# Optimization experiments

Measured on AMD Instinct MI355X. Metric: run time of the kernel, lower is better.

The kernel has to match this reference:

```python
import jax, jax.numpy as jnp
import numpy as np

NUM_HEADS = 8
NUM_LEVELS = 4
NUM_POINTS = 4


def setup_inputs() -> dict:
    key = jax.random.key(0)
    kq, kp, kv, k1, k2, k3, k4 = jax.random.split(key, 7)
    B, Q, C = 4, 4096, 256
    M, L, P = NUM_HEADS, NUM_LEVELS, NUM_POINTS
    shapes_np = np.array([[128, 128], [64, 64], [32, 32], [16, 16]], dtype=np.int32)
    sizes = shapes_np[:, 0] * shapes_np[:, 1]
    N = int(sizes.sum())  # 21760
    level_index = jnp.asarray(np.concatenate([[0], np.cumsum(sizes)[:-1]]).astype(np.int32))
    q = jax.random.normal(kq, (B, Q, C), jnp.float32)
    p = jax.random.uniform(kp, (B, Q, L, 2), jnp.float32)  # normalized ref points
    v = jax.random.normal(kv, (B, N, C), jnp.float32)
    # proj_offset bias: radial grid init from reset_parameters()
    t = np.arange(M, dtype=np.float32) * (2.0 * np.pi / M)
    grid = np.stack([np.cos(t), np.sin(t)], -1)
    grid = grid / np.abs(grid).max(-1, keepdims=True)
    grid = np.tile(grid[:, None, None, :], (1, L, P, 1)) * np.arange(1, P + 1, dtype=np.float32)[None, None, :, None]
    b_off = jnp.asarray(grid.reshape(-1))
    s = 1.0 / np.sqrt(C).astype(np.float32)
    W_off = jax.random.normal(k1, (C, M * L * P * 2), jnp.float32) * 0.01
    W_attn = jax.random.normal(k2, (C, M * L * P), jnp.float32) * s
    b_attn = jnp.zeros((M * L * P,), jnp.float32)
    W_val = jax.random.normal(k3, (C, C), jnp.float32) * s
    b_val = jnp.zeros((C,), jnp.float32)
    W_out = jax.random.normal(k4, (C, C), jnp.float32) * s
    b_out = jnp.zeros((C,), jnp.float32)
    return {"q": q, "p": p, "v": v, "shapes": jnp.asarray(shapes_np), "level_index": level_index,
            "W_off": W_off, "b_off": b_off, "W_attn": W_attn, "b_attn": b_attn,
            "W_val": W_val, "b_val": b_val, "W_out": W_out, "b_out": b_out}


def _ms_deform_attn(q, p, v, shapes, level_index, W_off, b_off, W_attn, b_attn, W_val, b_val, W_out, b_out):
    B, Q, C = q.shape
    M, L, P = NUM_HEADS, NUM_LEVELS, NUM_POINTS
    D = C // M
    N = v.shape[1]
    # value projection -> [B, M, N, D] (head-major for gather)
    v_p = (v @ W_val + b_val).reshape(B, N, M, D).transpose(0, 2, 1, 3)
    # attention weights, softmax over L*P (classic MSDeformAttn kernel contract)
    attn = jax.nn.softmax((q @ W_attn + b_attn).reshape(B, Q, M, L * P), axis=-1)
    attn = attn.reshape(B, Q, M, L, P)
    # sampling locations (P==2 reference-point branch)
    off = (q @ W_off + b_off).reshape(B, Q, M, L, P, 2)
    norm = jnp.stack([shapes[:, 1], shapes[:, 0]], -1).astype(jnp.float32)  # (W, H) per level
    loc = p[:, :, None, :, None, :] + off / norm[None, None, None, :, None, :]  # [B,Q,M,L,P,2]

    out = jnp.zeros((B, M, Q, D), jnp.float32)
    for l in range(L):
        Hf = shapes[l, 0].astype(jnp.float32)
        Wf = shapes[l, 1].astype(jnp.float32)
        Hi = shapes[l, 0]
        Wi = shapes[l, 1]
        base = level_index[l]
        # grid_sample(align_corners=False) convention: pixel = loc*size - 0.5
        x = loc[:, :, :, l, :, 0] * Wf - 0.5  # [B,Q,M,P]
        y = loc[:, :, :, l, :, 1] * Hf - 0.5
        x0 = jnp.floor(x)
        y0 = jnp.floor(y)
        lx, ly = x - x0, y - y0
        x0i = x0.astype(jnp.int32)
        y0i = y0.astype(jnp.int32)

        def corner(xi, yi, w):
            valid = (xi >= 0) & (xi < Wi) & (yi >= 0) & (yi < Hi)
            idx = base + jnp.clip(yi, 0, Hi - 1) * Wi + jnp.clip(xi, 0, Wi - 1)  # [B,Q,M,P]
            idx = idx.transpose(0, 2, 1, 3).reshape(B, M, Q * P)
            g = jnp.take_along_axis(v_p, idx[..., None], axis=2).reshape(B, M, Q, P, D)
            wv = (w * valid.astype(w.dtype)).transpose(0, 2, 1, 3)[..., None]  # [B,M,Q,P,1]
            return g * wv

        samp = (corner(x0i, y0i, (1 - lx) * (1 - ly))
                + corner(x0i + 1, y0i, lx * (1 - ly))
                + corner(x0i, y0i + 1, (1 - lx) * ly)
                + corner(x0i + 1, y0i + 1, lx * ly))  # [B,M,Q,P,D]
        a_l = attn[:, :, :, l, :].transpose(0, 2, 1, 3)  # [B,M,Q,P]
        out = out + jnp.einsum('bmqpd,bmqp->bmqd', samp, a_l)

    out = out.transpose(0, 2, 1, 3).reshape(B, Q, M * D)
    return out @ W_out + b_out


def reference(q, p, v, shapes, level_index, W_off, b_off, W_attn, b_attn, W_val, b_val, W_out, b_out):
    return _ms_deform_attn(q, p, v, shapes, level_index, W_off, b_off, W_attn, b_attn, W_val, b_val, W_out, b_out)
```

## Files before the change

### kernel.cpp

```cpp
#include <hip/hip_runtime.h>
#include <cstddef>

#define BB 4
#define QQ 4096
#define MM 8
#define NN 21760

typedef __bf16 bf16_8 __attribute__((ext_vector_type(8)));
typedef __bf16 bf16_4 __attribute__((ext_vector_type(4)));
typedef float  floatx4 __attribute__((ext_vector_type(4)));

__global__ __launch_bounds__(256) void prep_weights(
    const float* __restrict__ Wv, const float* __restrict__ Wa,
    const float* __restrict__ Wo, const float* __restrict__ Wu,
    const float* __restrict__ ba, const float* __restrict__ bo,
    __bf16* __restrict__ Wt, float* __restrict__ biasq)
{
    const int gid = blockIdx.x * 256 + threadIdx.x;
    if (gid < 65536) {
        const int n = gid >> 8, k = gid & 255;
        Wt[gid] = (__bf16)Wv[k * 256 + n];
    } else if (gid < 163840) {
        const int o = gid - 65536;
        const int n = o >> 8, k = o & 255;
        Wt[gid] = (__bf16)(n < 128 ? Wa[k * 128 + n] : Wo[k * 256 + (n - 128)]);
    } else if (gid < 229376) {
        const int o = gid - 163840;
        const int n = o >> 8, k = o & 255;
        Wt[gid] = (__bf16)Wu[k * 256 + n];
    } else if (gid < 229760) {
        const int j = gid - 229376;
        biasq[j] = (j < 128) ? ba[j] : bo[j - 128];
    }
}

template<typename AT, int NCOLS, int MODE, int TILES>
__global__ __launch_bounds__(512) void gemm_ws(
    const AT* __restrict__ A,
    const __bf16* __restrict__ Wn,
    const float* __restrict__ bias,
    void* __restrict__ Cout,
    int tokens, int ldc)
{
    constexpr int F  = NCOLS / 8;
    constexpr int NJ = F / 16;

    const int z = blockIdx.z;
    const AT* Ab = A + (size_t)z * tokens * 256;

    __shared__ __bf16 As[2][64][256];

    const int tid  = threadIdx.x;
    const int lane = tid & 63;
    const int wave = tid >> 6;
    const int quad = lane >> 4;
    const int l16  = lane & 15;
    const int wave_f = wave * F;

    bf16_8 wf[8][NJ];
    #pragma unroll
    for (int kk = 0; kk < 8; ++kk)
        #pragma unroll
        for (int j = 0; j < NJ; ++j)
            wf[kk][j] = *(const bf16_8*)(Wn + (size_t)(wave_f + j * 16 + l16) * 256
                                          + kk * 32 + quad * 8);

    const int tile0 = blockIdx.y * TILES;


    {
        const int token0 = tile0 * 64;
        if (sizeof(AT) == 4) {
            const float* Af = (const float*)Ab;
            #pragma unroll
            for (int h = 0; h < 2; ++h) {
                #pragma unroll
                for (int c = 0; c < 4; ++c) {
                    const int cid = c * 512 + tid;
                    const int r   = cid >> 5;
                    const int kc  = (cid & 31) * 4;
                    const int k   = h * 128 + kc;
                    const float4 av = *(const float4*)(Af + (size_t)(token0 + r) * 256 + k);
                    bf16_4 w;
                    w[0] = (__bf16)av.x; w[1] = (__bf16)av.y;
                    w[2] = (__bf16)av.z; w[3] = (__bf16)av.w;
                    const int col = ((((k >> 3) ^ (r & 7)) << 3) | (k & 7));
                    *(bf16_4*)&As[0][r][col] = w;
                }
            }
        } else {
            const __bf16* Ah = (const __bf16*)Ab;
            #pragma unroll
            for (int h = 0; h < 2; ++h) {
                #pragma unroll
                for (int c = 0; c < 2; ++c) {
                    const int cid = c * 512 + tid;
                    const int r   = cid >> 4;
                    const int kc  = (cid & 15) * 8;
                    const int k   = h * 128 + kc;
                    const bf16_8 av = *(const bf16_8*)(Ah + (size_t)(token0 + r) * 256 + k);
                    const int col = (((k >> 3) ^ (r & 7)) << 3);
                    *(bf16_8*)&As[0][r][col] = av;
                }
            }
        }
        __syncthreads();
    }

    #pragma unroll
    for (int t = 0; t < TILES; ++t) {
        const int cur    = t & 1;
        const int token0 = (tile0 + t) * 64;
        const bool more  = (t + 1 < TILES);
        const int ntok0  = token0 + 64;

        floatx4 acc[NJ][4] = {};

        float4 a4[4]; bf16_8 a8[2];
        if (more) {
            if (sizeof(AT) == 4) {
                const float* Af = (const float*)Ab;
                #pragma unroll
                for (int c = 0; c < 4; ++c) {
                    const int cid = c * 512 + tid;
                    const int r   = cid >> 5;
                    const int kc  = (cid & 31) * 4;
                    a4[c] = *(const float4*)(Af + (size_t)(ntok0 + r) * 256 + kc);
                }
            } else {
                const __bf16* Ah = (const __bf16*)Ab;
                #pragma unroll
                for (int c = 0; c < 2; ++c) {
                    const int cid = c * 512 + tid;
                    const int r   = cid >> 4;
                    const int kc  = (cid & 15) * 8;
                    a8[c] = *(const bf16_8*)(Ah + (size_t)(ntok0 + r) * 256 + kc);
                }
            }
        }

        #pragma unroll
        for (int kk = 0; kk < 4; ++kk) {
            bf16_8 af[4];
            #pragma unroll
            for (int it = 0; it < 4; ++it)
                af[it] = *(const bf16_8*)&As[cur][it * 16 + l16]
                                           [(((kk * 4 + quad) ^ (l16 & 7)) << 3)];
            #pragma unroll
            for (int j = 0; j < NJ; ++j)
                #pragma unroll
                for (int it = 0; it < 4; ++it)
                    acc[j][it] = __builtin_amdgcn_mfma_f32_16x16x32_bf16(wf[kk][j], af[it], acc[j][it], 0, 0, 0);
        }

        if (more) {
            if (sizeof(AT) == 4) {
                const float* Af = (const float*)Ab;
                #pragma unroll
                for (int c = 0; c < 4; ++c) {
                    const int cid = c * 512 + tid;
                    const int r   = cid >> 5;
                    const int kc  = (cid & 31) * 4;
                    bf16_4 w;
                    w[0] = (__bf16)a4[c].x; w[1] = (__bf16)a4[c].y;
                    w[2] = (__bf16)a4[c].z; w[3] = (__bf16)a4[c].w;
                    const int col = ((((kc >> 3) ^ (r & 7)) << 3) | (kc & 7));
                    *(bf16_4*)&As[cur ^ 1][r][col] = w;
                }
                #pragma unroll
                for (int c = 0; c < 4; ++c) {
                    const int cid = c * 512 + tid;
                    const int r   = cid >> 5;
                    const int kc  = (cid & 31) * 4;
                    a4[c] = *(const float4*)(Af + (size_t)(ntok0 + r) * 256 + 128 + kc);
                }
            } else {
                const __bf16* Ah = (const __bf16*)Ab;
                #pragma unroll
                for (int c = 0; c < 2; ++c) {
                    const int cid = c * 512 + tid;
                    const int r   = cid >> 4;
                    const int kc  = (cid & 15) * 8;
                    const int col = (((kc >> 3) ^ (r & 7)) << 3);
                    *(bf16_8*)&As[cur ^ 1][r][col] = a8[c];
                }
                #pragma unroll
                for (int c = 0; c < 2; ++c) {
                    const int cid = c * 512 + tid;
                    const int r   = cid >> 4;
                    const int kc  = (cid & 15) * 8;
                    a8[c] = *(const bf16_8*)(Ah + (size_t)(ntok0 + r) * 256 + 128 + kc);
                }
            }
        }

        #pragma unroll
        for (int kk = 4; kk < 8; ++kk) {
            bf16_8 af[4];
            #pragma unroll
            for (int it = 0; it < 4; ++it)
                af[it] = *(const bf16_8*)&As[cur][it * 16 + l16]
                                           [(((kk * 4 + quad) ^ (l16 & 7)) << 3)];
            #pragma unroll
            for (int j = 0; j < NJ; ++j)
                #pragma unroll
                for (int it = 0; it < 4; ++it)
                    acc[j][it] = __builtin_amdgcn_mfma_f32_16x16x32_bf16(wf[kk][j], af[it], acc[j][it], 0, 0, 0);
        }

        if (more) {
            if (sizeof(AT) == 4) {
                #pragma unroll
                for (int c = 0; c < 4; ++c) {
                    const int cid = c * 512 + tid;
                    const int r   = cid >> 5;
                    const int kc  = (cid & 31) * 4;
                    const int k   = 128 + kc;
                    bf16_4 w;
                    w[0] = (__bf16)a4[c].x; w[1] = (__bf16)a4[c].y;
                    w[2] = (__bf16)a4[c].z; w[3] = (__bf16)a4[c].w;
                    const int col = ((((k >> 3) ^ (r & 7)) << 3) | (k & 7));
                    *(bf16_4*)&As[cur ^ 1][r][col] = w;
                }
            } else {
                #pragma unroll
                for (int c = 0; c < 2; ++c) {
                    const int cid = c * 512 + tid;
                    const int r   = cid >> 4;
                    const int kc  = (cid & 15) * 8;
                    const int k   = 128 + kc;
                    const int col = (((k >> 3) ^ (r & 7)) << 3);
                    *(bf16_8*)&As[cur ^ 1][r][col] = a8[c];
                }
            }
        }

        #pragma unroll
        for (int j = 0; j < NJ; ++j) {
            const int n0 = wave_f + j * 16 + quad * 4;
            const float4 b4 = *(const float4*)(bias + n0);
            #pragma unroll
            for (int it = 0; it < 4; ++it) {
                const int token = token0 + it * 16 + l16;
                const float v0 = acc[j][it][0] + b4.x;
                const float v1 = acc[j][it][1] + b4.y;
                const float v2 = acc[j][it][2] + b4.z;
                const float v3 = acc[j][it][3] + b4.w;
                if (MODE == 0) {
                    float4 o; o.x = v0; o.y = v1; o.z = v2; o.w = v3;
                    *(float4*)((float*)Cout + ((size_t)z * tokens + token) * ldc + n0) = o;
                } else {
                    const int mh = n0 >> 5, dd = n0 & 31;
                    bf16_4 ob;
                    ob[0] = (__bf16)v0; ob[1] = (__bf16)v1; ob[2] = (__bf16)v2; ob[3] = (__bf16)v3;
                    *(bf16_4*)((__bf16*)Cout + (((size_t)z * 8 + mh) * NN + token) * 32 + dd) = ob;
                }
            }
        }

        if (more) __syncthreads();
    }
}

__device__ __forceinline__ float bflo(unsigned u) { return __uint_as_float(u << 16); }
__device__ __forceinline__ float bfhi(unsigned u) { return __uint_as_float(u & 0xffff0000u); }

__global__ __launch_bounds__(512) void sampler(
    const __bf16* __restrict__ vp,
    const float* __restrict__ gqp,
    const float* __restrict__ pref,
    __bf16* __restrict__ mid)
{
    const int t    = threadIdx.x;
    const int m    = t >> 6;
    const int lane = t & 63;
    const int s    = lane >> 2;
    const int c    = lane & 3;
    const int l    = s >> 2;
    const int bq   = blockIdx.x;
    const int b    = bq >> 12;

    const int   Hi = 128 >> l;
    const float Hf = (float)Hi;
    const int   base = (l == 0) ? 0 : (l == 1) ? 16384 : (l == 2) ? 20480 : 21504;

    const float logit = gqp[(size_t)bq * 384 + m * 16 + s];
    const float e = __expf(logit);
    float sum = e;
    #pragma unroll
    for (int k = 4; k < 64; k <<= 1) sum += __shfl_xor(sum, k, 64);
    const float a = e * __builtin_amdgcn_rcpf(sum);

    const float2 off = *(const float2*)(gqp + (size_t)bq * 384 + 128 + (m * 16 + s) * 2);
    const float2 pr  = *(const float2*)(pref + (size_t)bq * 8 + l * 2);

    const float x = fmaf(pr.x, Hf, off.x - 0.5f);
    const float y = fmaf(pr.y, Hf, off.y - 0.5f);
    const float x0f = floorf(x), y0f = floorf(y);
    const float lx = x - x0f, ly = y - y0f;
    const int x0 = (int)x0f, y0 = (int)y0f;
    const int cx0 = min(max(x0, 0), Hi - 1), cx1 = min(max(x0 + 1, 0), Hi - 1);
    const int cy0 = min(max(y0, 0), Hi - 1), cy1 = min(max(y0 + 1, 0), Hi - 1);
    const bool vx0 = (x0 >= 0) && (x0 < Hi), vx1 = (x0 + 1 >= 0) && (x0 + 1 < Hi);
    const bool vy0 = (y0 >= 0) && (y0 < Hi), vy1 = (y0 + 1 >= 0) && (y0 + 1 < Hi);
    const float w00 = a * (1.f - lx) * (1.f - ly) * ((vx0 && vy0) ? 1.f : 0.f);
    const float w10 = a * lx * (1.f - ly) * ((vx1 && vy0) ? 1.f : 0.f);
    const float w01 = a * (1.f - lx) * ly * ((vx0 && vy1) ? 1.f : 0.f);
    const float w11 = a * lx * ly * ((vx1 && vy1) ? 1.f : 0.f);

    const __bf16* vbase = vp + ((size_t)b * 8 + m) * NN * 32;
    const uint4 u00 = *((const uint4*)(vbase + (size_t)(base + cy0 * Hi + cx0) * 32) + c);
    const uint4 u10 = *((const uint4*)(vbase + (size_t)(base + cy0 * Hi + cx1) * 32) + c);
    const uint4 u01 = *((const uint4*)(vbase + (size_t)(base + cy1 * Hi + cx0) * 32) + c);
    const uint4 u11 = *((const uint4*)(vbase + (size_t)(base + cy1 * Hi + cx1) * 32) + c);

    float f[8];
    f[0] = w00*bflo(u00.x) + w10*bflo(u10.x) + w01*bflo(u01.x) + w11*bflo(u11.x);
    f[1] = w00*bfhi(u00.x) + w10*bfhi(u10.x) + w01*bfhi(u01.x) + w11*bfhi(u11.x);
    f[2] = w00*bflo(u00.y) + w10*bflo(u10.y) + w01*bflo(u01.y) + w11*bflo(u11.y);
    f[3] = w00*bfhi(u00.y) + w10*bfhi(u10.y) + w01*bfhi(u01.y) + w11*bfhi(u11.y);
    f[4] = w00*bflo(u00.z) + w10*bflo(u10.z) + w01*bflo(u01.z) + w11*bflo(u11.z);
    f[5] = w00*bfhi(u00.z) + w10*bfhi(u10.z) + w01*bfhi(u01.z) + w11*bfhi(u11.z);
    f[6] = w00*bflo(u00.w) + w10*bflo(u10.w) + w01*bflo(u01.w) + w11*bflo(u11.w);
    f[7] = w00*bfhi(u00.w) + w10*bfhi(u10.w) + w01*bfhi(u01.w) + w11*bfhi(u11.w);

    const int b2 = (lane >> 2) & 1, b3 = (lane >> 3) & 1, b4i = (lane >> 4) & 1;
    #pragma unroll
    for (int j = 0; j < 4; ++j) {
        const float sel  = b2 ? f[j] : f[j + 4];
        const float recv = __shfl_xor(sel, 4, 64);
        f[j] = (b2 ? f[j + 4] : f[j]) + recv;
    }
    #pragma unroll
    for (int j = 0; j < 2; ++j) {
        const float sel  = b3 ? f[j] : f[j + 2];
        const float recv = __shfl_xor(sel, 8, 64);
        f[j] = (b3 ? f[j + 2] : f[j]) + recv;
    }
    {
        const float sel  = b4i ? f[0] : f[1];
        const float recv = __shfl_xor(sel, 16, 64);
        f[0] = (b4i ? f[1] : f[0]) + recv;
    }
    f[0] += __shfl_xor(f[0], 32, 64);

    if (!(lane & 32)) {
        const int chan = (c << 3) | (b2 << 2) | (b3 << 1) | b4i;
        mid[(size_t)bq * 256 + m * 32 + chan] = (__bf16)f[0];
    }
}

extern "C" void kernel_launch(void* const* d_in, const int* in_sizes, int n_in,
                              void* d_out, int out_size, void* d_ws, size_t ws_size,
                              hipStream_t stream) {
    const float* q      = (const float*)d_in[0];
    const float* p      = (const float*)d_in[1];
    const float* v      = (const float*)d_in[2];
    const float* W_off  = (const float*)d_in[5];
    const float* b_off  = (const float*)d_in[6];
    const float* W_attn = (const float*)d_in[7];
    const float* b_attn = (const float*)d_in[8];
    const float* W_val  = (const float*)d_in[9];
    const float* b_val  = (const float*)d_in[10];
    const float* W_out  = (const float*)d_in[11];
    const float* b_out  = (const float*)d_in[12];
    float* out = (float*)d_out;

    float*  gqp   = (float*)d_ws;
    float*  biasq = gqp + (size_t)16384 * 384;
    __bf16* mid   = (__bf16*)(biasq + 384);
    __bf16* vpb   = mid + (size_t)16384 * 256;
    __bf16* Wt    = vpb + (size_t)BB * 8 * NN * 32;
    __bf16* Wt_val  = Wt;
    __bf16* Wt_attn = Wt + 65536;
    __bf16* Wt_off  = Wt + 65536 + 32768;
    __bf16* Wt_out  = Wt + 163840;

    prep_weights<<<898, 256, 0, stream>>>(W_val, W_attn, W_off, W_out, b_attn, b_off, Wt, biasq);

    {
        dim3 grid(1, 340 / 4, BB);
        gemm_ws<float, 256, 1, 4><<<grid, 512, 0, stream>>>(v, Wt_val, b_val, vpb, NN, 0);
    }
    {
        dim3 grid(1, 256, 1);
        gemm_ws<float, 128, 0, 1><<<grid, 512, 0, stream>>>(q, Wt_attn, biasq, gqp, BB * QQ, 384);
    }
    {
        dim3 grid(1, 256, 1);
        gemm_ws<float, 256, 0, 1><<<grid, 512, 0, stream>>>(q, Wt_off, biasq + 128, gqp + 128, BB * QQ, 384);
    }
    sampler<<<BB * QQ, 512, 0, stream>>>(vpb, gqp, p, mid);
    {
        dim3 grid(1, 256, 1);
        gemm_ws<__bf16, 256, 0, 1><<<grid, 512, 0, stream>>>(mid, Wt_out, b_out, out, BB * QQ, 256);
    }
}
```

Baseline: 252.7 us.

## Simplify GEMM to one tile per block, split columns across blocks, merge q projections

Drops the multi-tile double-buffered loop from the weight-stationary GEMM, so each block now handles one 64-token tile and a column slice chosen by blockIdx.x. The attention and offset projections of q become a single launch with three column blocks, and the output GEMM splits into two column blocks. Occupancy is raised with launch_bounds(512,4) and a single LDS buffer. The aim is more blocks, better occupancy and one fewer launch. The cost is that every block reloads its weight fragments, and A tiles are reread once per column block.

```diff
diff --git a/kernel.cpp b/kernel.cpp
--- a/kernel.cpp
+++ b/kernel.cpp
@@ -34,21 +34,23 @@
     }
 }
 
-template<typename AT, int NCOLS, int MODE, int TILES>
-__global__ __launch_bounds__(512) void gemm_ws(
+template<typename AT, int NCB, int MODE>
+__global__ __launch_bounds__(512, 4) void gemm_ws(
     const AT* __restrict__ A,
     const __bf16* __restrict__ Wn,
     const float* __restrict__ bias,
     void* __restrict__ Cout,
     int tokens, int ldc)
 {
-    constexpr int F  = NCOLS / 8;
+    constexpr int F  = NCB / 8;
     constexpr int NJ = F / 16;
 
-    const int z = blockIdx.z;
-    const AT* Ab = A + (size_t)z * tokens * 256;
-
-    __shared__ __bf16 As[2][64][256];
+    const int z    = blockIdx.z;
+    const int col0 = blockIdx.x * NCB;
+    const AT* Ab   = A + (size_t)z * tokens * 256;
+    const __bf16* Wb = Wn + (size_t)col0 * 256;
+
+    __shared__ __bf16 As[64][256];
 
     const int tid  = threadIdx.x;
     const int lane = tid & 63;
@@ -62,203 +64,74 @@
     for (int kk = 0; kk < 8; ++kk)
         #pragma unroll
         for (int j = 0; j < NJ; ++j)
-            wf[kk][j] = *(const bf16_8*)(Wn + (size_t)(wave_f + j * 16 + l16) * 256
+            wf[kk][j] = *(const bf16_8*)(Wb + (size_t)(wave_f + j * 16 + l16) * 256
                                           + kk * 32 + quad * 8);
 
-    const int tile0 = blockIdx.y * TILES;
-
-
-    {
-        const int token0 = tile0 * 64;
-        if (sizeof(AT) == 4) {
-            const float* Af = (const float*)Ab;
+    const int token0 = blockIdx.y * 64;
+    if (sizeof(AT) == 4) {
+        const float* Af = (const float*)Ab;
+        #pragma unroll
+        for (int c = 0; c < 8; ++c) {
+            const int cid = c * 512 + tid;
+            const int r   = cid >> 6;
+            const int kc  = (cid & 63) * 4;
+            const float4 av = *(const float4*)(Af + (size_t)(token0 + r) * 256 + kc);
+            bf16_4 w;
+            w[0] = (__bf16)av.x; w[1] = (__bf16)av.y;
+            w[2] = (__bf16)av.z; w[3] = (__bf16)av.w;
+            const int col = ((((kc >> 3) ^ (r & 7)) << 3) | (kc & 7));
+            *(bf16_4*)&As[r][col] = w;
+        }
+    } else {
+        const __bf16* Ah = (const __bf16*)Ab;
+        #pragma unroll
+        for (int c = 0; c < 4; ++c) {
+            const int cid = c * 512 + tid;
+            const int r   = cid >> 5;
+            const int kc  = (cid & 31) * 8;
+            const bf16_8 av = *(const bf16_8*)(Ah + (size_t)(token0 + r) * 256 + kc);
+            const int col = (((kc >> 3) ^ (r & 7)) << 3);
+            *(bf16_8*)&As[r][col] = av;
+        }
+    }
+    __syncthreads();
+
+    floatx4 acc[NJ][4] = {};
+    #pragma unroll
+    for (int kk = 0; kk < 8; ++kk) {
+        bf16_8 af[4];
+        #pragma unroll
+        for (int it = 0; it < 4; ++it)
+            af[it] = *(const bf16_8*)&As[it * 16 + l16]
+                                       [(((kk * 4 + quad) ^ (l16 & 7)) << 3)];
+        #pragma unroll
+        for (int j = 0; j < NJ; ++j)
             #pragma unroll
-            for (int h = 0; h < 2; ++h) {
-                #pragma unroll
-                for (int c = 0; c < 4; ++c) {
-                    const int cid = c * 512 + tid;
-                    const int r   = cid >> 5;
-                    const int kc  = (cid & 31) * 4;
-                    const int k   = h * 128 + kc;
-                    const float4 av = *(const float4*)(Af + (size_t)(token0 + r) * 256 + k);
-                    bf16_4 w;
-                    w[0] = (__bf16)av.x; w[1] = (__bf16)av.y;
-                    w[2] = (__bf16)av.z; w[3] = (__bf16)av.w;
-                    const int col = ((((k >> 3) ^ (r & 7)) << 3) | (k & 7));
-                    *(bf16_4*)&As[0][r][col] = w;
-                }
-            }
-        } else {
-            const __bf16* Ah = (const __bf16*)Ab;
-            #pragma unroll
-            for (int h = 0; h < 2; ++h) {
-                #pragma unroll
-                for (int c = 0; c < 2; ++c) {
-                    const int cid = c * 512 + tid;
-                    const int r   = cid >> 4;
-                    const int kc  = (cid & 15) * 8;
-                    const int k   = h * 128 + kc;
-                    const bf16_8 av = *(const bf16_8*)(Ah + (size_t)(token0 + r) * 256 + k);
-                    const int col = (((k >> 3) ^ (r & 7)) << 3);
-                    *(bf16_8*)&As[0][r][col] = av;
-                }
+            for (int it = 0; it < 4; ++it)
+                acc[j][it] = __builtin_amdgcn_mfma_f32_16x16x32_bf16(wf[kk][j], af[it], acc[j][it], 0, 0, 0);
+    }
+
+    #pragma unroll
+    for (int j = 0; j < NJ; ++j) {
+        const int n0 = col0 + wave_f + j * 16 + quad * 4;
+        const float4 b4 = *(const float4*)(bias + n0);
+        #pragma unroll
+        for (int it = 0; it < 4; ++it) {
+            const int token = token0 + it * 16 + l16;
+            const float v0 = acc[j][it][0] + b4.x;
+            const float v1 = acc[j][it][1] + b4.y;
+            const float v2 = acc[j][it][2] + b4.z;
+            const float v3 = acc[j][it][3] + b4.w;
+            if (MODE == 0) {
+                float4 o; o.x = v0; o.y = v1; o.z = v2; o.w = v3;
+                *(float4*)((float*)Cout + ((size_t)z * tokens + token) * ldc + n0) = o;
+            } else {
+                const int mh = n0 >> 5, dd = n0 & 31;
+                bf16_4 ob;
+                ob[0] = (__bf16)v0; ob[1] = (__bf16)v1; ob[2] = (__bf16)v2; ob[3] = (__bf16)v3;
+                *(bf16_4*)((__bf16*)Cout + (((size_t)z * 8 + mh) * NN + token) * 32 + dd) = ob;
             }
         }
-        __syncthreads();
-    }
-
-    #pragma unroll
-    for (int t = 0; t < TILES; ++t) {
-        const int cur    = t & 1;
-        const int token0 = (tile0 + t) * 64;
-        const bool more  = (t + 1 < TILES);
-        const int ntok0  = token0 + 64;
-
-        floatx4 acc[NJ][4] = {};
-
-        float4 a4[4]; bf16_8 a8[2];
-        if (more) {
-            if (sizeof(AT) == 4) {
-                const float* Af = (const float*)Ab;
-                #pragma unroll
-                for (int c = 0; c < 4; ++c) {
-                    const int cid = c * 512 + tid;
-                    const int r   = cid >> 5;
-                    const int kc  = (cid & 31) * 4;
-                    a4[c] = *(const float4*)(Af + (size_t)(ntok0 + r) * 256 + kc);
-                }
-            } else {
-                const __bf16* Ah = (const __bf16*)Ab;
-                #pragma unroll
-                for (int c = 0; c < 2; ++c) {
-                    const int cid = c * 512 + tid;
-                    const int r   = cid >> 4;
-                    const int kc  = (cid & 15) * 8;
-                    a8[c] = *(const bf16_8*)(Ah + (size_t)(ntok0 + r) * 256 + kc);
-                }
-            }
-        }
-
-        #pragma unroll
-        for (int kk = 0; kk < 4; ++kk) {
-            bf16_8 af[4];
-            #pragma unroll
-            for (int it = 0; it < 4; ++it)
-                af[it] = *(const bf16_8*)&As[cur][it * 16 + l16]
-                                           [(((kk * 4 + quad) ^ (l16 & 7)) << 3)];
-            #pragma unroll
-            for (int j = 0; j < NJ; ++j)
-                #pragma unroll
-                for (int it = 0; it < 4; ++it)
-                    acc[j][it] = __builtin_amdgcn_mfma_f32_16x16x32_bf16(wf[kk][j], af[it], acc[j][it], 0, 0, 0);
-        }
-
-        if (more) {
-            if (sizeof(AT) == 4) {
-                const float* Af = (const float*)Ab;
-                #pragma unroll
-                for (int c = 0; c < 4; ++c) {
-                    const int cid = c * 512 + tid;
-                    const int r   = cid >> 5;
-                    const int kc  = (cid & 31) * 4;
-                    bf16_4 w;
-                    w[0] = (__bf16)a4[c].x; w[1] = (__bf16)a4[c].y;
-                    w[2] = (__bf16)a4[c].z; w[3] = (__bf16)a4[c].w;
-                    const int col = ((((kc >> 3) ^ (r & 7)) << 3) | (kc & 7));
-                    *(bf16_4*)&As[cur ^ 1][r][col] = w;
-                }
-                #pragma unroll
-                for (int c = 0; c < 4; ++c) {
-                    const int cid = c * 512 + tid;
-                    const int r   = cid >> 5;
-                    const int kc  = (cid & 31) * 4;
-                    a4[c] = *(const float4*)(Af + (size_t)(ntok0 + r) * 256 + 128 + kc);
-                }
-            } else {
-                const __bf16* Ah = (const __bf16*)Ab;
-                #pragma unroll
-                for (int c = 0; c < 2; ++c) {
-                    const int cid = c * 512 + tid;
-                    const int r   = cid >> 4;
-                    const int kc  = (cid & 15) * 8;
-                    const int col = (((kc >> 3) ^ (r & 7)) << 3);
-                    *(bf16_8*)&As[cur ^ 1][r][col] = a8[c];
-                }
-                #pragma unroll
-                for (int c = 0; c < 2; ++c) {
-                    const int cid = c * 512 + tid;
-                    const int r   = cid >> 4;
-                    const int kc  = (cid & 15) * 8;
-                    a8[c] = *(const bf16_8*)(Ah + (size_t)(ntok0 + r) * 256 + 128 + kc);
-                }
-            }
-        }
-
-        #pragma unroll
-        for (int kk = 4; kk < 8; ++kk) {
-            bf16_8 af[4];
-            #pragma unroll
-            for (int it = 0; it < 4; ++it)
-                af[it] = *(const bf16_8*)&As[cur][it * 16 + l16]
-                                           [(((kk * 4 + quad) ^ (l16 & 7)) << 3)];
-            #pragma unroll
-            for (int j = 0; j < NJ; ++j)
-                #pragma unroll
-                for (int it = 0; it < 4; ++it)
-                    acc[j][it] = __builtin_amdgcn_mfma_f32_16x16x32_bf16(wf[kk][j], af[it], acc[j][it], 0, 0, 0);
-        }
-
-        if (more) {
-            if (sizeof(AT) == 4) {
-                #pragma unroll
-                for (int c = 0; c < 4; ++c) {
-                    const int cid = c * 512 + tid;
-                    const int r   = cid >> 5;
-                    const int kc  = (cid & 31) * 4;
-                    const int k   = 128 + kc;
-                    bf16_4 w;
-                    w[0] = (__bf16)a4[c].x; w[1] = (__bf16)a4[c].y;
-                    w[2] = (__bf16)a4[c].z; w[3] = (__bf16)a4[c].w;
-                    const int col = ((((k >> 3) ^ (r & 7)) << 3) | (k & 7));
-                    *(bf16_4*)&As[cur ^ 1][r][col] = w;
-                }
-            } else {
-                #pragma unroll
-                for (int c = 0; c < 2; ++c) {
-                    const int cid = c * 512 + tid;
-                    const int r   = cid >> 4;
-                    const int kc  = (cid & 15) * 8;
-                    const int k   = 128 + kc;
-                    const int col = (((k >> 3) ^ (r & 7)) << 3);
-                    *(bf16_8*)&As[cur ^ 1][r][col] = a8[c];
-                }
-            }
-        }
-
-        #pragma unroll
-        for (int j = 0; j < NJ; ++j) {
-            const int n0 = wave_f + j * 16 + quad * 4;
-            const float4 b4 = *(const float4*)(bias + n0);
-            #pragma unroll
-            for (int it = 0; it < 4; ++it) {
-                const int token = token0 + it * 16 + l16;
-                const float v0 = acc[j][it][0] + b4.x;
-                const float v1 = acc[j][it][1] + b4.y;
-                const float v2 = acc[j][it][2] + b4.z;
-                const float v3 = acc[j][it][3] + b4.w;
-                if (MODE == 0) {
-                    float4 o; o.x = v0; o.y = v1; o.z = v2; o.w = v3;
-                    *(float4*)((float*)Cout + ((size_t)z * tokens + token) * ldc + n0) = o;
-                } else {
-                    const int mh = n0 >> 5, dd = n0 & 31;
-                    bf16_4 ob;
-                    ob[0] = (__bf16)v0; ob[1] = (__bf16)v1; ob[2] = (__bf16)v2; ob[3] = (__bf16)v3;
-                    *(bf16_4*)((__bf16*)Cout + (((size_t)z * 8 + mh) * NN + token) * 32 + dd) = ob;
-                }
-            }
-        }
-
-        if (more) __syncthreads();
     }
 }
 
@@ -371,28 +244,23 @@
     __bf16* mid   = (__bf16*)(biasq + 384);
     __bf16* vpb   = mid + (size_t)16384 * 256;
     __bf16* Wt    = vpb + (size_t)BB * 8 * NN * 32;
-    __bf16* Wt_val  = Wt;
-    __bf16* Wt_attn = Wt + 65536;
-    __bf16* Wt_off  = Wt + 65536 + 32768;
-    __bf16* Wt_out  = Wt + 163840;
+    __bf16* Wt_val = Wt;
+    __bf16* Wt_q   = Wt + 65536;
+    __bf16* Wt_out = Wt + 163840;
 
     prep_weights<<<898, 256, 0, stream>>>(W_val, W_attn, W_off, W_out, b_attn, b_off, Wt, biasq);
 
     {
-        dim3 grid(1, 340 / 4, BB);
-        gemm_ws<float, 256, 1, 4><<<grid, 512, 0, stream>>>(v, Wt_val, b_val, vpb, NN, 0);
-    }
-    {
-        dim3 grid(1, 256, 1);
-        gemm_ws<float, 128, 0, 1><<<grid, 512, 0, stream>>>(q, Wt_attn, biasq, gqp, BB * QQ, 384);
-    }
-    {
-        dim3 grid(1, 256, 1);
-        gemm_ws<float, 256, 0, 1><<<grid, 512, 0, stream>>>(q, Wt_off, biasq + 128, gqp + 128, BB * QQ, 384);
+        dim3 grid(1, 340, BB);
+        gemm_ws<float, 256, 1><<<grid, 512, 0, stream>>>(v, Wt_val, b_val, vpb, NN, 0);
+    }
+    {
+        dim3 grid(3, 256, 1);
+        gemm_ws<float, 128, 0><<<grid, 512, 0, stream>>>(q, Wt_q, biasq, gqp, BB * QQ, 384);
     }
     sampler<<<BB * QQ, 512, 0, stream>>>(vpb, gqp, p, mid);
     {
-        dim3 grid(1, 256, 1);
-        gemm_ws<__bf16, 256, 0, 1><<<grid, 512, 0, stream>>>(mid, Wt_out, b_out, out, BB * QQ, 256);
-    }
-}
+        dim3 grid(2, 256, 1);
+        gemm_ws<__bf16, 128, 0><<<grid, 512, 0, stream>>>(mid, Wt_out, b_out, out, BB * QQ, 256);
+    }
+}
```

Result: faster. 246.6 us (-2.4%).
